# Kernel optimization log

Hardware: AMD Instinct MI355X
Metric: run time of the kernel (lower is better)

The kernel has to match this reference:

```python
import jax, jax.numpy as jnp
import numpy as np

BATCH, IN, OUT, P = 8192, 1024, 1024, 8

def setup_inputs() -> dict:
    key = jax.random.key(0)
    k1, k2, k3 = jax.random.split(key, 3)
    x = jax.random.normal(k1, (BATCH, IN), dtype=jnp.float32)
    # per-(output,input) basis coefficients, init ~ randn*0.1 as in torch module
    coefficients = jax.random.normal(k2, (OUT, IN, P), dtype=jnp.float32) * 0.1
    weights = jax.random.normal(k3, (OUT, IN), dtype=jnp.float32)
    return {"x": x, "coefficients": coefficients, "weights": weights}

def reference(x, coefficients, weights):
    # out[b,o] = sum_i x[b,i] * (sum_p coef[o,i,p]) * weights[o,i]
    # == x @ (coef_sum * weights)^T  -- single fused GEMM
    w_eff = coefficients.sum(axis=-1) * weights  # [O, I]
    return jnp.einsum('bi,oi->bo', x, w_eff)
```

## Files before the change

### kernel.cpp

```cpp
#include <hip/hip_runtime.h>
#include <hip/hip_bf16.h>
#include <stdint.h>

#define BATCH 8192
#define IN    1024
#define OUTD  1024
#define PBASIS 8

typedef __attribute__((ext_vector_type(8))) short bf16x8;
typedef __attribute__((ext_vector_type(4))) float floatx4;

__device__ __forceinline__ unsigned short f2bf(float f) {
    union { float f; unsigned u; } v; v.f = f;
    unsigned u = v.u;
    u += 0x7fffu + ((u >> 16) & 1u);
    return (unsigned short)(u >> 16);
}

__global__ void prep_kernel(const float* __restrict__ x,
                            const float* __restrict__ coef,
                            const float* __restrict__ w,
                            unsigned short* __restrict__ xb,
                            unsigned short* __restrict__ weff) {
    int b = blockIdx.x;
    int tid = threadIdx.x;
    if (b < 4096) {
        int idx = b * 256 + tid;
        const float4* p = (const float4*)(x + (size_t)idx * 8);
        float4 a = p[0], c = p[1];
        uint4 o;
        o.x = (unsigned)f2bf(a.x) | ((unsigned)f2bf(a.y) << 16);
        o.y = (unsigned)f2bf(a.z) | ((unsigned)f2bf(a.w) << 16);
        o.z = (unsigned)f2bf(c.x) | ((unsigned)f2bf(c.y) << 16);
        o.w = (unsigned)f2bf(c.z) | ((unsigned)f2bf(c.w) << 16);
        ((uint4*)xb)[idx] = o;
    } else {
        int idx = (b - 4096) * 256 + tid;
        size_t e0 = (size_t)idx * 2;
        const float4* c4 = (const float4*)(coef + e0 * PBASIS);
        float4 a = c4[0], bb = c4[1], c = c4[2], d = c4[3];
        float s0 = (a.x + a.y + a.z + a.w) + (bb.x + bb.y + bb.z + bb.w);
        float s1 = (c.x + c.y + c.z + c.w) + (d.x + d.y + d.z + d.w);
        float2 ww = ((const float2*)w)[idx];
        unsigned b0 = f2bf(s0 * ww.x);
        unsigned b1 = f2bf(s1 * ww.y);
        ((unsigned*)weff)[idx] = b0 | (b1 << 16);
    }
}

__global__ __launch_bounds__(256, 3) void gemm_bt(
        const unsigned short* __restrict__ A,
        const unsigned short* __restrict__ B,
        float* __restrict__ C) {
    constexpr int K = IN, BK = 64;
    constexpr int ES = 132;
    __shared__ __align__(16) char smem[32768];
    unsigned short* As = (unsigned short*)smem;
    unsigned short* Bs = As + 128 * BK;
    float* ebuf = (float*)smem;

    const int tid  = threadIdx.x;
    const int bm   = blockIdx.x, bn = blockIdx.y;
    const int lane = tid & 63;
    const int wave = tid >> 6;
    const int wm   = wave & 1, wn = wave >> 1;
    const int t    = lane & 15;
    const int q    = lane >> 4;
    const int r8   = t & 7;

    const char* gA[4]; const char* gB[4];
    void* lA[4]; void* lB[4];
#pragma unroll
    for (int j = 0; j < 4; ++j) {
        int L = j * 256 + tid;
        int row = L >> 3;
        int cg  = (L & 7) ^ (row & 7);
        gA[j] = (const char*)(A + ((size_t)(bm * 128 + row)) * K + cg * 8);
        gB[j] = (const char*)(B + ((size_t)(bn * 128 + row)) * K + cg * 8);
        lA[j] = (void*)(As + (size_t)L * 8);
        lB[j] = (void*)(Bs + (size_t)L * 8);
    }

    const unsigned short* aB0 = As + (wm * 64 + t) * BK + ((0 + q) ^ r8) * 8;
    const unsigned short* aB1 = As + (wm * 64 + t) * BK + ((4 + q) ^ r8) * 8;
    const unsigned short* bB0 = Bs + (wn * 64 + t) * BK + ((0 + q) ^ r8) * 8;
    const unsigned short* bB1 = Bs + (wn * 64 + t) * BK + ((4 + q) ^ r8) * 8;

    floatx4 acc[4][4];
#pragma unroll
    for (int i = 0; i < 4; ++i)
#pragma unroll
        for (int j = 0; j < 4; ++j)
            acc[i][j] = (floatx4){0.f, 0.f, 0.f, 0.f};

    for (int k0 = 0; k0 < K; k0 += BK) {
#pragma unroll
        for (int j = 0; j < 4; ++j) {
            __builtin_amdgcn_global_load_lds(
                (const __attribute__((address_space(1))) unsigned*)gA[j],
                (__attribute__((address_space(3))) unsigned*)lA[j], 16, 0, 0);
            __builtin_amdgcn_global_load_lds(
                (const __attribute__((address_space(1))) unsigned*)gB[j],
                (__attribute__((address_space(3))) unsigned*)lB[j], 16, 0, 0);
            gA[j] += BK * 2;
            gB[j] += BK * 2;
        }
        __syncthreads();

        bf16x8 af[2][4], bfv[2][4];
#pragma unroll
        for (int i = 0; i < 4; ++i) {
            af[0][i]  = *(const bf16x8*)(aB0 + i * 1024);
            af[1][i]  = *(const bf16x8*)(aB1 + i * 1024);
            bfv[0][i] = *(const bf16x8*)(bB0 + i * 1024);
            bfv[1][i] = *(const bf16x8*)(bB1 + i * 1024);
        }
#pragma unroll
        for (int i = 0; i < 4; ++i)
#pragma unroll
            for (int j = 0; j < 4; ++j) {
                acc[i][j] = __builtin_amdgcn_mfma_f32_16x16x32_bf16(
                    af[0][i], bfv[0][j], acc[i][j], 0, 0, 0);
                acc[i][j] = __builtin_amdgcn_mfma_f32_16x16x32_bf16(
                    af[1][i], bfv[1][j], acc[i][j], 0, 0, 0);
            }
        __syncthreads();
    }

#pragma unroll
    for (int p = 0; p < 4; ++p) {
        if (p) __syncthreads();
        if (wm == (p >> 1)) {
            int dt = p & 1;
#pragma unroll
            for (int half = 0; half < 2; ++half) {
                int tm = dt * 2 + half;
#pragma unroll
                for (int tn = 0; tn < 4; ++tn) {
                    int col = wn * 64 + tn * 16 + t;
#pragma unroll
                    for (int r = 0; r < 4; ++r) {
                        int brow = half * 16 + q * 4 + r;
                        ebuf[brow * ES + col] = acc[tm][tn][r];
                    }
                }
            }
        }
        __syncthreads();
#pragma unroll
        for (int rr = 0; rr < 4; ++rr) {
            int brow = rr * 8 + (tid >> 5);
            int col4 = tid & 31;
            float4 v = *(const float4*)(ebuf + brow * ES + col4 * 4);
            size_t grow = (size_t)(bm * 128 + p * 32 + brow);
            *(float4*)(C + grow * OUTD + bn * 128 + col4 * 4) = v;
        }
    }
}

extern "C" void kernel_launch(void* const* d_in, const int* in_sizes, int n_in,
                              void* d_out, int out_size, void* d_ws, size_t ws_size,
                              hipStream_t stream) {
    const float* x    = (const float*)d_in[0];
    const float* coef = (const float*)d_in[1];
    const float* w    = (const float*)d_in[2];
    float* out = (float*)d_out;

    unsigned short* xb   = (unsigned short*)d_ws;
    unsigned short* weff = (unsigned short*)((char*)d_ws + (size_t)BATCH * IN * 2);

    prep_kernel<<<6144, 256, 0, stream>>>(x, coef, w, xb, weff);
    gemm_bt<<<dim3(BATCH / 128, OUTD / 128), 256, 0, stream>>>(xb, weff, out);
}
```

Baseline: 125.6 us.

## Register-prefetch next K tile instead of direct global-to-LDS loads

Replaces the synchronous global_load_lds copy of each K tile with a register-staged software pipeline. The next tile's global loads are issued into registers before the current tile is stored to LDS and computed, so load latency can overlap with MFMA work. The swizzle moves from the global side to the LDS store side. More live registers are needed, so the occupancy hint drops from 3 to 2 blocks per SIMD, and one redundant wrapped load is issued on the last iteration.

```diff
diff --git a/kernel.cpp b/kernel.cpp
--- a/kernel.cpp
+++ b/kernel.cpp
@@ -48,7 +48,7 @@
     }
 }
 
-__global__ __launch_bounds__(256, 3) void gemm_bt(
+__global__ __launch_bounds__(256, 2) void gemm_bt(
         const unsigned short* __restrict__ A,
         const unsigned short* __restrict__ B,
         float* __restrict__ C) {
@@ -68,17 +68,18 @@
     const int q    = lane >> 4;
     const int r8   = t & 7;
 
-    const char* gA[4]; const char* gB[4];
-    void* lA[4]; void* lB[4];
+    const unsigned short* gA[4]; const unsigned short* gB[4];
+    unsigned short* lA[4]; unsigned short* lB[4];
 #pragma unroll
     for (int j = 0; j < 4; ++j) {
-        int L = j * 256 + tid;
-        int row = L >> 3;
-        int cg  = (L & 7) ^ (row & 7);
-        gA[j] = (const char*)(A + ((size_t)(bm * 128 + row)) * K + cg * 8);
-        gB[j] = (const char*)(B + ((size_t)(bn * 128 + row)) * K + cg * 8);
-        lA[j] = (void*)(As + (size_t)L * 8);
-        lB[j] = (void*)(Bs + (size_t)L * 8);
+        int G   = j * 256 + tid;
+        int row = G >> 3;
+        int c   = G & 7;
+        int sl  = row * 8 + (c ^ (row & 7));
+        gA[j] = A + (size_t)(bm * 128 + row) * K + c * 8;
+        gB[j] = B + (size_t)(bn * 128 + row) * K + c * 8;
+        lA[j] = As + sl * 8;
+        lB[j] = Bs + sl * 8;
     }
 
     const unsigned short* aB0 = As + (wm * 64 + t) * BK + ((0 + q) ^ r8) * 8;
@@ -93,39 +94,59 @@
         for (int j = 0; j < 4; ++j)
             acc[i][j] = (floatx4){0.f, 0.f, 0.f, 0.f};
 
-    for (int k0 = 0; k0 < K; k0 += BK) {
-#pragma unroll
-        for (int j = 0; j < 4; ++j) {
-            __builtin_amdgcn_global_load_lds(
-                (const __attribute__((address_space(1))) unsigned*)gA[j],
-                (__attribute__((address_space(3))) unsigned*)lA[j], 16, 0, 0);
-            __builtin_amdgcn_global_load_lds(
-                (const __attribute__((address_space(1))) unsigned*)gB[j],
-                (__attribute__((address_space(3))) unsigned*)lB[j], 16, 0, 0);
-            gA[j] += BK * 2;
-            gB[j] += BK * 2;
-        }
+    uint4 ra[4], rb[4], na[4], nb[4];
+
+#define LOADT(RA, RB, KOFF)                                         \
+    _Pragma("unroll")                                               \
+    for (int j = 0; j < 4; ++j) {                                   \
+        RA[j] = *(const uint4*)(gA[j] + (KOFF));                    \
+        RB[j] = *(const uint4*)(gB[j] + (KOFF));                    \
+    }
+
+#define STORET(RA, RB)                                              \
+    _Pragma("unroll")                                               \
+    for (int j = 0; j < 4; ++j) {                                   \
+        *(uint4*)lA[j] = RA[j];                                     \
+        *(uint4*)lB[j] = RB[j];                                     \
+    }
+
+#define COMPUTE()                                                   \
+    {                                                               \
+        bf16x8 af[2][4], bfv[2][4];                                 \
+        _Pragma("unroll")                                           \
+        for (int i = 0; i < 4; ++i) {                               \
+            af[0][i]  = *(const bf16x8*)(aB0 + i * 1024);           \
+            af[1][i]  = *(const bf16x8*)(aB1 + i * 1024);           \
+            bfv[0][i] = *(const bf16x8*)(bB0 + i * 1024);           \
+            bfv[1][i] = *(const bf16x8*)(bB1 + i * 1024);           \
+        }                                                           \
+        _Pragma("unroll")                                           \
+        for (int i = 0; i < 4; ++i)                                 \
+            _Pragma("unroll")                                       \
+            for (int j = 0; j < 4; ++j) {                           \
+                acc[i][j] = __builtin_amdgcn_mfma_f32_16x16x32_bf16(\
+                    af[0][i], bfv[0][j], acc[i][j], 0, 0, 0);       \
+                acc[i][j] = __builtin_amdgcn_mfma_f32_16x16x32_bf16(\
+                    af[1][i], bfv[1][j], acc[i][j], 0, 0, 0);       \
+            }                                                       \
+    }
+
+    LOADT(ra, rb, 0);
+    for (int k0 = 0; k0 < K; k0 += 2 * BK) {
+        LOADT(na, nb, k0 + BK);
+        STORET(ra, rb);
         __syncthreads();
-
-        bf16x8 af[2][4], bfv[2][4];
-#pragma unroll
-        for (int i = 0; i < 4; ++i) {
-            af[0][i]  = *(const bf16x8*)(aB0 + i * 1024);
-            af[1][i]  = *(const bf16x8*)(aB1 + i * 1024);
-            bfv[0][i] = *(const bf16x8*)(bB0 + i * 1024);
-            bfv[1][i] = *(const bf16x8*)(bB1 + i * 1024);
-        }
-#pragma unroll
-        for (int i = 0; i < 4; ++i)
-#pragma unroll
-            for (int j = 0; j < 4; ++j) {
-                acc[i][j] = __builtin_amdgcn_mfma_f32_16x16x32_bf16(
-                    af[0][i], bfv[0][j], acc[i][j], 0, 0, 0);
-                acc[i][j] = __builtin_amdgcn_mfma_f32_16x16x32_bf16(
-                    af[1][i], bfv[1][j], acc[i][j], 0, 0, 0);
-            }
+        COMPUTE();
+        __syncthreads();
+        LOADT(ra, rb, (k0 + 2 * BK) & (K - 1));
+        STORET(na, nb);
+        __syncthreads();
+        COMPUTE();
         __syncthreads();
     }
+#undef LOADT
+#undef STORET
+#undef COMPUTE
 
 #pragma unroll
     for (int p = 0; p < 4; ++p) {
```

After: 213.8 us. +70.2%, slower.
